# Optimization experiments

Measured on AMD Instinct MI355X. Metric: run time of the kernel, lower is better.

## Reference

```python
import jax, jax.numpy as jnp
import numpy as np

B, N, K = 8, 512, 16            # batches, proposals per batch, knn neighbors
C_POOL = 256                    # pooled feature dim (hardcoded 256 in source)
G_MLP = [128, 128]              # GLOBAL_INFORMATION.MLP_LAYERS
IN_DIM = C_POOL + G_MLP[-1]     # gnn_input_dim = 384
LAYERS = [512, 512, 512]


def _xavier(key, shape):
    fan_out, fan_in = shape
    lim = np.sqrt(6.0 / (fan_in + fan_out))
    return jax.random.uniform(key, shape, jnp.float32, -lim, lim)


def setup_inputs() -> dict:
    key = jax.random.key(0)
    ks = jax.random.split(key, 12)
    rois = jax.random.normal(ks[0], (B, N, 7), jnp.float32)
    rois = rois.at[:, :, :3].multiply(20.0)  # spread box centers spatially
    pooled_features = jax.random.normal(ks[1], (B, N, C_POOL), jnp.float32)

    # knn_graph per batch (loop=False): edges (neighbor j -> center i)
    coords = rois[:, :, :3]
    d2 = jnp.sum((coords[:, :, None, :] - coords[:, None, :, :]) ** 2, -1)  # [B,N,N]
    d2 = d2 + jnp.eye(N, dtype=jnp.float32) * 1e9                           # no self loops
    _, nbr = jax.lax.top_k(-d2, K)                                          # [B,N,K]
    offs = (jnp.arange(B) * N)[:, None, None]
    src = (nbr + offs).reshape(-1)
    dst = (jnp.broadcast_to(jnp.arange(N)[None, :, None], (B, N, K)) + offs).reshape(-1)
    edge_index = jnp.stack([src, dst]).astype(jnp.int32)                    # [2, B*N*K]

    # global-information MLP params: Linear(7,128), Linear(128,128)
    gW1 = _xavier(ks[2], (G_MLP[0], 7)); gb1 = jnp.zeros((G_MLP[0],), jnp.float32)
    gW2 = _xavier(ks[3], (G_MLP[1], G_MLP[0])); gb2 = jnp.zeros((G_MLP[1],), jnp.float32)

    # EdgeConv fc params: in = 2*in_dim of layer
    fcW1 = _xavier(ks[4], (LAYERS[0], 2 * IN_DIM)); fcb1 = jnp.zeros((LAYERS[0],), jnp.float32)
    fcW2 = _xavier(ks[5], (LAYERS[1], 2 * LAYERS[0])); fcb2 = jnp.zeros((LAYERS[1],), jnp.float32)
    fcW3 = _xavier(ks[6], (LAYERS[2], 2 * LAYERS[1])); fcb3 = jnp.zeros((LAYERS[2],), jnp.float32)

    return dict(rois=rois, pooled_features=pooled_features, edge_index=edge_index,
                gW1=gW1, gb1=gb1, gW2=gW2, gb2=gb2,
                fcW1=fcW1, fcb1=fcb1, fcW2=fcW2, fcb2=fcb2, fcW3=fcW3, fcb3=fcb3)


def reference(rois, pooled_features, edge_index,
              gW1, gb1, gW2, gb2,
              fcW1, fcb1, fcW2, fcb2, fcW3, fcb3):
    # global information MLP on proposal boxes
    g = jax.nn.relu(rois @ gW1.T + gb1)
    g = jax.nn.relu(g @ gW2.T + gb2)                      # [B,N,128]
    x = jnp.concatenate([pooled_features, g], -1).reshape(-1, IN_DIM)  # [B*N, 384]

    src, dst = edge_index[0], edge_index[1]
    n_nodes = B * N
    feats = [x]
    for W, b in ((fcW1, fcb1), (fcW2, fcb2), (fcW3, fcb3)):
        x_i = x[dst]                                      # target features [E,d]
        x_j = x[src]                                      # source features [E,d]
        msg = jax.nn.relu(jnp.concatenate([x_j - x_i, x_i], -1) @ W.T + b)  # [E,out]
        x = jax.ops.segment_max(msg, dst, num_segments=n_nodes)  # scatter-max aggr
        feats.append(x)
    return jnp.concatenate(feats, -1)                     # [B*N, 384+512*3]
```

## Files before the change

### kernel.cpp

```cpp
#include <hip/hip_runtime.h>
#include <hip/hip_bf16.h>

#define BN_NODES 4096
#define KNN 16
#define C_POOL 256
#define G_DIM 128
#define IN_DIM 384
#define L_DIM 512
#define OUT_STRIDE 1920

#define X1_OFF 384
#define X2_OFF 896
#define X3_OFF 1408

typedef __attribute__((ext_vector_type(8))) __bf16 bf16x8;
typedef __attribute__((ext_vector_type(4))) float floatx4;
typedef __attribute__((ext_vector_type(8))) unsigned short ushortx8;

static __device__ __forceinline__ ushort f2bf(float v) {
  return __builtin_bit_cast(ushort, __float2bfloat16(v));
}
static __device__ __forceinline__ float bf2f(ushort u) {
  return __builtin_bit_cast(float, ((unsigned)u) << 16);
}
static __device__ __forceinline__ void gld_lds(const ushort* g, ushort* l) {
  __builtin_amdgcn_global_load_lds(
      (const __attribute__((address_space(1))) void*)g,
      (__attribute__((address_space(3))) void*)l, 16, 0, 0);
}

__global__ __launch_bounds__(256) void prep_kernel(
    const float* __restrict__ rois, const float* __restrict__ pooled,
    const float* __restrict__ gW1, const float* __restrict__ gb1,
    const float* __restrict__ gW2, const float* __restrict__ gb2,
    const float* __restrict__ W0, const float* __restrict__ W1,
    const float* __restrict__ W2, float* __restrict__ out,
    ushort* __restrict__ Xb0, ushort* __restrict__ Wb0,
    ushort* __restrict__ Wb1, ushort* __restrict__ Wb2) {
  const int t = threadIdx.x;
  if (blockIdx.x >= 512) {
    int wi = blockIdx.x - 512;
    const float* W;
    ushort* Wb;
    int K, base;
    if (wi < 384) {
      W = W0; Wb = Wb0; K = IN_DIM; base = wi;
    } else if (wi < 896) {
      W = W1; Wb = Wb1; K = L_DIM; base = wi - 384;
    } else {
      W = W2; Wb = Wb2; K = L_DIM; base = wi - 896;
    }
    int elem = base * 1024 + t * 4;
    int j = elem / K;
    int k = elem - j * K;
    const float* srcp = (j < 512) ? W + (size_t)j * (2 * K) + k
                                  : W + (size_t)(j - 512) * (2 * K) + K + k;
    ushort4 pk;
    pk.x = f2bf(srcp[0]);
    pk.y = f2bf(srcp[1]);
    pk.z = f2bf(srcp[2]);
    pk.w = f2bf(srcp[3]);
    *(ushort4*)(Wb + (size_t)j * K + k) = pk;
    return;
  }
  const int nb = blockIdx.x * 8;
  const int c = t & 127;
  const int nh = t >> 7;
  __shared__ float rs[8 * 7];
  __shared__ __align__(16) float h1[8][G_DIM];
  if (t < 56) rs[t] = rois[(size_t)nb * 7 + t];
  __syncthreads();
  {
    float w1[7];
#pragma unroll
    for (int i = 0; i < 7; i++) w1[i] = gW1[c * 7 + i];
    float b1 = gb1[c];
#pragma unroll
    for (int n = nh * 4; n < nh * 4 + 4; n++) {
      float a = b1;
#pragma unroll
      for (int i = 0; i < 7; i++) a += rs[n * 7 + i] * w1[i];
      h1[n][c] = fmaxf(a, 0.f);
    }
  }
  __syncthreads();
  float acc[4];
  {
    float b2 = gb2[c];
#pragma unroll
    for (int n = 0; n < 4; n++) acc[n] = b2;
    const float4* w4 = (const float4*)(gW2 + (size_t)c * G_DIM);
#pragma unroll 4
    for (int kc = 0; kc < G_DIM / 4; kc++) {
      float4 wv = w4[kc];
#pragma unroll
      for (int n = 0; n < 4; n++) {
        float4 hv = ((const float4*)h1[nh * 4 + n])[kc];
        acc[n] += wv.x * hv.x + wv.y * hv.y + wv.z * hv.z + wv.w * hv.w;
      }
    }
  }
#pragma unroll
  for (int n = 0; n < 4; n++) {
    int node = nb + nh * 4 + n;
    float g = fmaxf(acc[n], 0.f);
    const float* prow = pooled + (size_t)node * C_POOL;
    float p0 = prow[c], p1 = prow[G_DIM + c];
    float* orow = out + (size_t)node * OUT_STRIDE;
    orow[c] = p0;
    orow[G_DIM + c] = p1;
    orow[C_POOL + c] = g;
    ushort* xrow = Xb0 + (size_t)node * IN_DIM;
    xrow[c] = f2bf(p0);
    xrow[G_DIM + c] = f2bf(p1);
    xrow[C_POOL + c] = f2bf(g);
  }
}

template <int K>
__global__ __launch_bounds__(512) void mfma_gemm_kernel(
    const ushort* __restrict__ Xb, const ushort* __restrict__ Wb,
    ushort* __restrict__ PQb) {
  __shared__ __align__(16) ushort sA[128 * 64];
  __shared__ __align__(16) ushort sB[64 * 64];
  const int tid = threadIdx.x;
  const int lane = tid & 63;
  const int w = tid >> 6;
  const int wm = w >> 1;
  const int wn = w & 1;
  const int fr = lane & 15;
  const int kc = lane >> 4;
  const int bm = blockIdx.x, bn = blockIdx.y;

  floatx4 acc[2][2];
#pragma unroll
  for (int i = 0; i < 2; i++)
#pragma unroll
    for (int j = 0; j < 2; j++) acc[i][j] = (floatx4){0.f, 0.f, 0.f, 0.f};

#pragma unroll
  for (int k0 = 0; k0 < K; k0 += 64) {
#pragma unroll
    for (int r = 0; r < 2; r++) {
      int ta = w + r * 8;
      int rt = ta >> 1, ks = ta & 1;
      const ushort* ga =
          Xb + (size_t)(bm * 128 + rt * 16 + fr) * K + k0 + ks * 32 + kc * 8;
      gld_lds(ga, &sA[ta * 512 + lane * 8]);
    }
    {
      int ct = w >> 1, ks = w & 1;
      const ushort* gb =
          Wb + (size_t)(bn * 64 + ct * 16 + fr) * K + k0 + ks * 32 + kc * 8;
      gld_lds(gb, &sB[w * 512 + lane * 8]);
    }
    __syncthreads();
#pragma unroll
    for (int ks = 0; ks < 2; ks++) {
      bf16x8 af[2], bf[2];
#pragma unroll
      for (int i = 0; i < 2; i++)
        af[i] = *(const bf16x8*)&sA[((wm * 2 + i) * 2 + ks) * 512 + lane * 8];
#pragma unroll
      for (int j = 0; j < 2; j++)
        bf[j] = *(const bf16x8*)&sB[((wn * 2 + j) * 2 + ks) * 512 + lane * 8];
#pragma unroll
      for (int i = 0; i < 2; i++)
#pragma unroll
        for (int j = 0; j < 2; j++)
          acc[i][j] = __builtin_amdgcn_mfma_f32_16x16x32_bf16(af[i], bf[j],
                                                              acc[i][j], 0, 0,
                                                              0);
    }
    __syncthreads();
  }

  const int rowB = bm * 128 + wm * 32 + kc * 4;
  const int colB = bn * 64 + wn * 32 + fr;
#pragma unroll
  for (int i = 0; i < 2; i++)
#pragma unroll
    for (int j = 0; j < 2; j++)
#pragma unroll
      for (int r = 0; r < 4; r++)
        PQb[(size_t)(rowB + i * 16 + r) * 1024 + colB + j * 16] =
            f2bf(acc[i][j][r]);
}

__global__ __launch_bounds__(512) void edge_kernel(
    const ushort* __restrict__ PQb, const int* __restrict__ src,
    const float* __restrict__ bias, float* __restrict__ out, int out_off,
    ushort* __restrict__ Xb, int write_x) {
  const int n = blockIdx.x * 8 + (threadIdx.x >> 6);
  const int l = threadIdx.x & 63;

  int nbr[KNN];
  {
    const int4* sp = (const int4*)(src + (size_t)n * KNN);
#pragma unroll
    for (int k4 = 0; k4 < 4; k4++) {
      int4 v = sp[k4];
      nbr[k4 * 4 + 0] = v.x;
      nbr[k4 * 4 + 1] = v.y;
      nbr[k4 * 4 + 2] = v.z;
      nbr[k4 * 4 + 3] = v.w;
    }
  }

  const ushort* own = PQb + (size_t)n * 1024 + l * 8;
  ushortx8 pu = *(const ushortx8*)own;
  ushortx8 qu = *(const ushortx8*)(own + 512);

  float m[8];
#pragma unroll
  for (int c = 0; c < 8; c++) m[c] = -1e30f;
#pragma unroll
  for (int k = 0; k < KNN; k++) {
    ushortx8 u = *(const ushortx8*)(PQb + (size_t)nbr[k] * 1024 + l * 8);
#pragma unroll
    for (int c = 0; c < 8; c++) m[c] = fmaxf(m[c], bf2f(u[c]));
  }

  const float4 bb0 = *(const float4*)&bias[l * 8];
  const float4 bb1 = *(const float4*)&bias[l * 8 + 4];
  float res[8];
#pragma unroll
  for (int c = 0; c < 8; c++) {
    float bbv = (c < 4) ? ((const float*)&bb0)[c] : ((const float*)&bb1)[c - 4];
    res[c] = fmaxf(m[c] - bf2f(pu[c]) + bf2f(qu[c]) + bbv, 0.f);
  }

  float* orow = out + (size_t)n * OUT_STRIDE + out_off + l * 8;
  *(float4*)orow = (float4){res[0], res[1], res[2], res[3]};
  *(float4*)(orow + 4) = (float4){res[4], res[5], res[6], res[7]};
  if (write_x) {
    ushortx8 pk;
#pragma unroll
    for (int c = 0; c < 8; c++) pk[c] = f2bf(res[c]);
    *(ushortx8*)(Xb + (size_t)n * L_DIM + l * 8) = pk;
  }
}

extern "C" void kernel_launch(void* const* d_in, const int* in_sizes, int n_in,
                              void* d_out, int out_size, void* d_ws,
                              size_t ws_size, hipStream_t stream) {
  const float* rois = (const float*)d_in[0];
  const float* pooled = (const float*)d_in[1];
  const int* edge_index = (const int*)d_in[2];
  const float* gW1 = (const float*)d_in[3];
  const float* gb1 = (const float*)d_in[4];
  const float* gW2 = (const float*)d_in[5];
  const float* gb2 = (const float*)d_in[6];
  const float* fcW[3] = {(const float*)d_in[7], (const float*)d_in[9],
                         (const float*)d_in[11]};
  const float* fcb[3] = {(const float*)d_in[8], (const float*)d_in[10],
                         (const float*)d_in[12]};
  float* out = (float*)d_out;
  const int* src = edge_index;

  char* ws = (char*)d_ws;
  ushort* PQb = (ushort*)ws;
  ushort* Xb = (ushort*)(ws + (size_t)8 * 1024 * 1024);
  ushort* Wb[3] = {(ushort*)(ws + (size_t)12 * 1024 * 1024),
                   (ushort*)(ws + (size_t)13 * 1024 * 1024),
                   (ushort*)(ws + (size_t)14 * 1024 * 1024)};

  prep_kernel<<<1920, 256, 0, stream>>>(rois, pooled, gW1, gb1, gW2, gb2,
                                        fcW[0], fcW[1], fcW[2], out, Xb, Wb[0],
                                        Wb[1], Wb[2]);

  mfma_gemm_kernel<IN_DIM><<<dim3(32, 16), 512, 0, stream>>>(Xb, Wb[0], PQb);
  edge_kernel<<<512, 512, 0, stream>>>(PQb, src, fcb[0], out, X1_OFF, Xb, 1);
  mfma_gemm_kernel<L_DIM><<<dim3(32, 16), 512, 0, stream>>>(Xb, Wb[1], PQb);
  edge_kernel<<<512, 512, 0, stream>>>(PQb, src, fcb[1], out, X2_OFF, Xb, 1);
  mfma_gemm_kernel<L_DIM><<<dim3(32, 16), 512, 0, stream>>>(Xb, Wb[2], PQb);
  edge_kernel<<<512, 512, 0, stream>>>(PQb, src, fcb[2], out, X3_OFF, Xb, 0);
}
```

Baseline: 169.5 us.

## Double-buffer GEMM LDS tiles and remap edge kernel blocks across batches

The MFMA GEMM now keeps two LDS buffers for the A and B tiles and issues the global-to-LDS loads for the next K tile before computing on the current one. This aims to hide global load latency behind MFMA work, at the cost of doubling shared memory per block, which may lower occupancy. The edge kernel also remaps block IDs so that consecutive blocks go to different batches (bid&7 picks the batch), spreading neighbor gathers across the 8 batch regions. That remap may change cache or XCD locality, either for better or worse.

After: 167.1 us. About the same (-1.4%).

```diff
diff --git a/kernel.cpp b/kernel.cpp
--- a/kernel.cpp
+++ b/kernel.cpp
@@ -121,8 +121,8 @@
 __global__ __launch_bounds__(512) void mfma_gemm_kernel(
     const ushort* __restrict__ Xb, const ushort* __restrict__ Wb,
     ushort* __restrict__ PQb) {
-  __shared__ __align__(16) ushort sA[128 * 64];
-  __shared__ __align__(16) ushort sB[64 * 64];
+  __shared__ __align__(16) ushort sA[2][128 * 64];
+  __shared__ __align__(16) ushort sB[2][64 * 64];
   const int tid = threadIdx.x;
   const int lane = tid & 63;
   const int w = tid >> 6;
@@ -131,6 +131,15 @@
   const int fr = lane & 15;
   const int kc = lane >> 4;
   const int bm = blockIdx.x, bn = blockIdx.y;
+  constexpr int NT = K / 64;
+
+  const int ta0 = w, ta1 = w + 8;
+  const int rt0 = ta0 >> 1, ks0 = ta0 & 1;
+  const int rt1 = ta1 >> 1, ks1 = ta1 & 1;
+  const int ctB = w >> 1, ksB = w & 1;
+  const ushort* gA0 = Xb + (size_t)(bm * 128 + rt0 * 16 + fr) * K + ks0 * 32 + kc * 8;
+  const ushort* gA1 = Xb + (size_t)(bm * 128 + rt1 * 16 + fr) * K + ks1 * 32 + kc * 8;
+  const ushort* gB = Wb + (size_t)(bn * 64 + ctB * 16 + fr) * K + ksB * 32 + kc * 8;
 
   floatx4 acc[2][2];
 #pragma unroll
@@ -138,37 +147,36 @@
 #pragma unroll
     for (int j = 0; j < 2; j++) acc[i][j] = (floatx4){0.f, 0.f, 0.f, 0.f};
 
-#pragma unroll
-  for (int k0 = 0; k0 < K; k0 += 64) {
-#pragma unroll
-    for (int r = 0; r < 2; r++) {
-      int ta = w + r * 8;
-      int rt = ta >> 1, ks = ta & 1;
-      const ushort* ga =
-          Xb + (size_t)(bm * 128 + rt * 16 + fr) * K + k0 + ks * 32 + kc * 8;
-      gld_lds(ga, &sA[ta * 512 + lane * 8]);
-    }
-    {
-      int ct = w >> 1, ks = w & 1;
-      const ushort* gb =
-          Wb + (size_t)(bn * 64 + ct * 16 + fr) * K + k0 + ks * 32 + kc * 8;
-      gld_lds(gb, &sB[w * 512 + lane * 8]);
-    }
-    __syncthreads();
+  gld_lds(gA0, &sA[0][ta0 * 512 + lane * 8]);
+  gld_lds(gA1, &sA[0][ta1 * 512 + lane * 8]);
+  gld_lds(gB, &sB[0][w * 512 + lane * 8]);
+  __syncthreads();
+
+#pragma unroll
+  for (int t = 0; t < NT; ++t) {
+    const int cur = t & 1;
+    if (t + 1 < NT) {
+      const int k0n = (t + 1) * 64;
+      gld_lds(gA0 + k0n, &sA[cur ^ 1][ta0 * 512 + lane * 8]);
+      gld_lds(gA1 + k0n, &sA[cur ^ 1][ta1 * 512 + lane * 8]);
+      gld_lds(gB + k0n, &sB[cur ^ 1][w * 512 + lane * 8]);
+    }
 #pragma unroll
     for (int ks = 0; ks < 2; ks++) {
-      bf16x8 af[2], bf[2];
+      bf16x8 af[2], bfr[2];
 #pragma unroll
       for (int i = 0; i < 2; i++)
-        af[i] = *(const bf16x8*)&sA[((wm * 2 + i) * 2 + ks) * 512 + lane * 8];
+        af[i] =
+            *(const bf16x8*)&sA[cur][((wm * 2 + i) * 2 + ks) * 512 + lane * 8];
 #pragma unroll
       for (int j = 0; j < 2; j++)
-        bf[j] = *(const bf16x8*)&sB[((wn * 2 + j) * 2 + ks) * 512 + lane * 8];
+        bfr[j] =
+            *(const bf16x8*)&sB[cur][((wn * 2 + j) * 2 + ks) * 512 + lane * 8];
 #pragma unroll
       for (int i = 0; i < 2; i++)
 #pragma unroll
         for (int j = 0; j < 2; j++)
-          acc[i][j] = __builtin_amdgcn_mfma_f32_16x16x32_bf16(af[i], bf[j],
+          acc[i][j] = __builtin_amdgcn_mfma_f32_16x16x32_bf16(af[i], bfr[j],
                                                               acc[i][j], 0, 0,
                                                               0);
     }
@@ -191,7 +199,8 @@
     const ushort* __restrict__ PQb, const int* __restrict__ src,
     const float* __restrict__ bias, float* __restrict__ out, int out_off,
     ushort* __restrict__ Xb, int write_x) {
-  const int n = blockIdx.x * 8 + (threadIdx.x >> 6);
+  const int bid = blockIdx.x;
+  const int n = (bid & 7) * 512 + (bid >> 3) * 8 + (threadIdx.x >> 6);
   const int l = threadIdx.x & 63;
 
   int nbr[KNN];
```
